# Performance work log

Measured on AMD Instinct MI355X. Metric: run time of the kernel, lower is better.

## Reference

```python
import jax, jax.numpy as jnp
import numpy as np

NUM_GRAPHS = 64
MAX_NODES = 512
D_MODEL = 512


def _lengths():
    # deterministic variable graph sizes in [256, 512]
    return 256 + (np.arange(NUM_GRAPHS) * 7) % 257


def setup_inputs() -> dict:
    key = jax.random.key(0)
    lengths = _lengths()
    total = int(lengths.sum())  # 23557
    # per-node graph id and within-graph position (replaces torch.split + pad_sequence)
    graph_ids = np.repeat(np.arange(NUM_GRAPHS, dtype=np.int32), lengths)
    pos_ids = np.concatenate([np.arange(n, dtype=np.int32) for n in lengths])
    batched_h = jax.random.normal(key, (total, D_MODEL), dtype=jnp.float32)
    return {
        "batched_h": batched_h,
        "graph_ids": jnp.asarray(graph_ids),
        "pos_ids": jnp.asarray(pos_ids),
        "B": NUM_GRAPHS,
        "max_n": MAX_NODES,
    }


def reference(batched_h, graph_ids, pos_ids, B, max_n):
    # pad_sequence equivalent: scatter nodes into [B, max_n, D] zero-padded tensor
    D = batched_h.shape[-1]
    padded = jnp.zeros((B, max_n, D), dtype=batched_h.dtype)
    padded = padded.at[graph_ids, pos_ids].set(batched_h)
    # Wq = Wk = Identity; bmm(q, k^T) -> [B, max_n, max_n]
    inst_out = jnp.einsum("bnd,bmd->bnm", padded, padded)
    # return_feat=False -> feat_out is empty; return inst_out only
    return inst_out
```

## Files before the change

kernel.cpp:

```cpp
#include <hip/hip_runtime.h>
#include <hip/hip_bf16.h>

#define DCONST 512
#define MAXN   512
#define NGRAPH 64

typedef __bf16 bf16x8 __attribute__((ext_vector_type(8)));
typedef float  f32x4  __attribute__((ext_vector_type(4)));
typedef float  fvec4  __attribute__((ext_vector_type(4)));

__global__ void pad_convert(const float* __restrict__ h,
                            __bf16* __restrict__ padded)
{
    const int t   = blockIdx.x * blockDim.x + threadIdx.x;
    const int row = t >> 6;
    const int seg = t & 63;
    const int g   = row >> 9;
    const int p   = row & 511;

    int off = 0, m7 = 0;
    for (int i = 0; i < g; ++i) {
        off += 256 + m7;
        m7 += 7; if (m7 >= 257) m7 -= 257;
    }
    const int len = 256 + m7;

    bf16x8 v = {};
    if (p < len) {
        const fvec4* src = reinterpret_cast<const fvec4*>(
            h + (size_t)(off + p) * DCONST + seg * 8);
        fvec4 a = src[0];
        fvec4 b = src[1];
        v[0] = (__bf16)a[0]; v[1] = (__bf16)a[1]; v[2] = (__bf16)a[2]; v[3] = (__bf16)a[3];
        v[4] = (__bf16)b[0]; v[5] = (__bf16)b[1]; v[6] = (__bf16)b[2]; v[7] = (__bf16)b[3];
    }
    *reinterpret_cast<bf16x8*>(padded + (size_t)row * DCONST + seg * 8) = v;
}

__constant__ const int TI10[10] = {0,0,0,0,1,1,1,2,2,3};
__constant__ const int TJ10[10] = {0,1,2,3,1,2,3,2,3,3};

__global__ __launch_bounds__(256, 2) void gemm_xxt(const __bf16* __restrict__ X,
                                                   float* __restrict__ out)
{
    __shared__ __align__(16) __bf16 lds[2][2][128][64];

    const int bid = blockIdx.x;
    const int xcd = bid & 7;
    const int idx = bid >> 3;
    const int g   = xcd * 8 + idx / 10;
    const int tl  = idx % 10;
    const int ti  = TI10[tl];
    const int tj  = TJ10[tl];
    const bool diag = (ti == tj);
    const int row0 = ti * 128;
    const int col0 = tj * 128;

    const __bf16* __restrict__ Xg = X + (size_t)g * MAXN * DCONST;

    const int tid  = threadIdx.x;
    const int wave = tid >> 6;
    const int lane = tid & 63;
    const int wr   = wave >> 1;
    const int wc   = wave & 1;

    f32x4 acc[4][4] = {};

    const int srow  = lane >> 3;
    const int sslot = lane & 7;

    auto stage = [&](int buf, int kt) {
        const int k0 = kt * 64;
        #pragma unroll
        for (int r = 0; r < 4; ++r) {
            const int rbase = wave * 8 + r * 32;
            const int rr    = rbase + srow;
            const int chunk = sslot ^ (rr & 7);
            const __bf16* gA = Xg + (size_t)(row0 + rr) * DCONST + k0 + chunk * 8;
            __builtin_amdgcn_global_load_lds(gA, &lds[buf][0][rbase][0], 16, 0, 0);
            if (!diag) {
                const __bf16* gB = Xg + (size_t)(col0 + rr) * DCONST + k0 + chunk * 8;
                __builtin_amdgcn_global_load_lds(gB, &lds[buf][1][rbase][0], 16, 0, 0);
            }
        }
    };

    stage(0, 0);
    asm volatile("s_waitcnt vmcnt(0)" ::: "memory");
    __syncthreads();

    int cur = 0;
    const int fr = lane & 15;
    const int q  = lane >> 4;
    const int bb = diag ? 0 : 1;

    #pragma unroll
    for (int kt = 0; kt < 8; ++kt) {
        if (kt < 7) stage(cur ^ 1, kt + 1);

        bf16x8 afr[2][4], bfr[2][4];
        #pragma unroll
        for (int ks = 0; ks < 2; ++ks) {
            const int chunk = ks * 4 + q;
            #pragma unroll
            for (int m = 0; m < 4; ++m) {
                const int rr   = wr * 64 + m * 16 + fr;
                const int slot = chunk ^ (rr & 7);
                afr[ks][m] = *reinterpret_cast<const bf16x8*>(&lds[cur][0][rr][slot * 8]);
            }
            #pragma unroll
            for (int n = 0; n < 4; ++n) {
                const int rr   = wc * 64 + n * 16 + fr;
                const int slot = chunk ^ (rr & 7);
                bfr[ks][n] = *reinterpret_cast<const bf16x8*>(&lds[cur][bb][rr][slot * 8]);
            }
        }

        #pragma unroll
        for (int ks = 0; ks < 2; ++ks)
            #pragma unroll
            for (int m = 0; m < 4; ++m)
                #pragma unroll
                for (int n = 0; n < 4; ++n)
                    acc[m][n] = __builtin_amdgcn_mfma_f32_16x16x32_bf16(
                        afr[ks][m], bfr[ks][n], acc[m][n], 0, 0, 0);

        if (kt < 7) {
            asm volatile("s_waitcnt vmcnt(0)" ::: "memory");
            __syncthreads();
        }
        cur ^= 1;
    }

    float* __restrict__ og = out + (size_t)g * MAXN * MAXN;
    const int rl0 = wr * 64 + q * 4;
    const int cl0 = wc * 64 + fr;
    #pragma unroll
    for (int m = 0; m < 4; ++m) {
        #pragma unroll
        for (int n = 0; n < 4; ++n) {
            f32x4 v = acc[m][n];
            float* p = og + (size_t)(row0 + rl0 + m * 16) * MAXN + col0 + cl0 + n * 16;
            #pragma unroll
            for (int r = 0; r < 4; ++r)
                p[(size_t)r * MAXN] = v[r];
            if (!diag) {
                float* pT = og + (size_t)(col0 + cl0 + n * 16) * MAXN
                               + row0 + rl0 + m * 16;
                *reinterpret_cast<f32x4*>(pT) = v;
            }
        }
    }
}

extern "C" void kernel_launch(void* const* d_in, const int* in_sizes, int n_in,
                              void* d_out, int out_size, void* d_ws, size_t ws_size,
                              hipStream_t stream)
{
    const float* h   = (const float*)d_in[0];
    __bf16* padded   = (__bf16*)d_ws;
    float*  out      = (float*)d_out;

    const int rows = NGRAPH * MAXN;
    pad_convert<<<rows * 64 / 256, 256, 0, stream>>>(h, padded);

    gemm_xxt<<<dim3(NGRAPH * 10), dim3(256), 0, stream>>>(padded, out);
}
```

Before: 126.8 us.

## Fuse ragged pad and bf16 conversion into the Gram GEMM kernel

Removes the separate pad_convert kernel and the bf16 padded workspace. The GEMM now loads fp32 rows directly from the ragged input into registers, zero-filling rows past each graph's length, then converts them to bf16 and writes them to swizzled LDS for the next k-tile. This eliminates an intermediate global write/read and a kernel launch. In exchange, staging goes through registers instead of direct global-to-LDS loads, which raises register pressure, and the fp32 input is re-read by multiple tiles.

```diff
diff --git a/kernel.cpp b/kernel.cpp
--- a/kernel.cpp
+++ b/kernel.cpp
@@ -9,39 +9,11 @@
 typedef float  f32x4  __attribute__((ext_vector_type(4)));
 typedef float  fvec4  __attribute__((ext_vector_type(4)));
 
-__global__ void pad_convert(const float* __restrict__ h,
-                            __bf16* __restrict__ padded)
-{
-    const int t   = blockIdx.x * blockDim.x + threadIdx.x;
-    const int row = t >> 6;
-    const int seg = t & 63;
-    const int g   = row >> 9;
-    const int p   = row & 511;
-
-    int off = 0, m7 = 0;
-    for (int i = 0; i < g; ++i) {
-        off += 256 + m7;
-        m7 += 7; if (m7 >= 257) m7 -= 257;
-    }
-    const int len = 256 + m7;
-
-    bf16x8 v = {};
-    if (p < len) {
-        const fvec4* src = reinterpret_cast<const fvec4*>(
-            h + (size_t)(off + p) * DCONST + seg * 8);
-        fvec4 a = src[0];
-        fvec4 b = src[1];
-        v[0] = (__bf16)a[0]; v[1] = (__bf16)a[1]; v[2] = (__bf16)a[2]; v[3] = (__bf16)a[3];
-        v[4] = (__bf16)b[0]; v[5] = (__bf16)b[1]; v[6] = (__bf16)b[2]; v[7] = (__bf16)b[3];
-    }
-    *reinterpret_cast<bf16x8*>(padded + (size_t)row * DCONST + seg * 8) = v;
-}
-
 __constant__ const int TI10[10] = {0,0,0,0,1,1,1,2,2,3};
 __constant__ const int TJ10[10] = {0,1,2,3,1,2,3,2,3,3};
 
-__global__ __launch_bounds__(256, 2) void gemm_xxt(const __bf16* __restrict__ X,
-                                                   float* __restrict__ out)
+__global__ __launch_bounds__(256, 2) void gram_fused(const float* __restrict__ h,
+                                                     float* __restrict__ out)
 {
     __shared__ __align__(16) __bf16 lds[2][2][128][64];
 
@@ -56,7 +28,12 @@
     const int row0 = ti * 128;
     const int col0 = tj * 128;
 
-    const __bf16* __restrict__ Xg = X + (size_t)g * MAXN * DCONST;
+    int off = 0, m7 = 0;
+    for (int i = 0; i < g; ++i) {
+        off += 256 + m7;
+        m7 += 7; if (m7 >= 257) m7 -= 257;
+    }
+    const int len = 256 + m7;
 
     const int tid  = threadIdx.x;
     const int wave = tid >> 6;
@@ -64,29 +41,67 @@
     const int wr   = wave >> 1;
     const int wc   = wave & 1;
 
+    const int slot = tid & 7;
+    const int rq   = tid >> 3;
+
     f32x4 acc[4][4] = {};
 
-    const int srow  = lane >> 3;
-    const int sslot = lane & 7;
+    fvec4 la[4][2], lb[4][2];
 
-    auto stage = [&](int buf, int kt) {
+    auto issue_loads = [&](int kt) {
         const int k0 = kt * 64;
         #pragma unroll
         for (int r = 0; r < 4; ++r) {
-            const int rbase = wave * 8 + r * 32;
-            const int rr    = rbase + srow;
-            const int chunk = sslot ^ (rr & 7);
-            const __bf16* gA = Xg + (size_t)(row0 + rr) * DCONST + k0 + chunk * 8;
-            __builtin_amdgcn_global_load_lds(gA, &lds[buf][0][rbase][0], 16, 0, 0);
+            const int rr = rq + r * 32;
+            const int ra = row0 + rr;
+            if (ra < len) {
+                const fvec4* s = reinterpret_cast<const fvec4*>(
+                    h + (size_t)(off + ra) * DCONST + k0 + slot * 8);
+                la[r][0] = s[0];
+                la[r][1] = s[1];
+            } else {
+                la[r][0] = (fvec4){0.f, 0.f, 0.f, 0.f};
+                la[r][1] = (fvec4){0.f, 0.f, 0.f, 0.f};
+            }
             if (!diag) {
-                const __bf16* gB = Xg + (size_t)(col0 + rr) * DCONST + k0 + chunk * 8;
-                __builtin_amdgcn_global_load_lds(gB, &lds[buf][1][rbase][0], 16, 0, 0);
+                const int rb = col0 + rr;
+                if (rb < len) {
+                    const fvec4* s = reinterpret_cast<const fvec4*>(
+                        h + (size_t)(off + rb) * DCONST + k0 + slot * 8);
+                    lb[r][0] = s[0];
+                    lb[r][1] = s[1];
+                } else {
+                    lb[r][0] = (fvec4){0.f, 0.f, 0.f, 0.f};
+                    lb[r][1] = (fvec4){0.f, 0.f, 0.f, 0.f};
+                }
             }
         }
     };
 
-    stage(0, 0);
-    asm volatile("s_waitcnt vmcnt(0)" ::: "memory");
+    auto write_tiles = [&](int buf) {
+        #pragma unroll
+        for (int r = 0; r < 4; ++r) {
+            const int rr = rq + r * 32;
+            const int sl = (slot ^ (rr & 7)) * 8;
+            bf16x8 v;
+            v[0] = (__bf16)la[r][0][0]; v[1] = (__bf16)la[r][0][1];
+            v[2] = (__bf16)la[r][0][2]; v[3] = (__bf16)la[r][0][3];
+            v[4] = (__bf16)la[r][1][0]; v[5] = (__bf16)la[r][1][1];
+            v[6] = (__bf16)la[r][1][2]; v[7] = (__bf16)la[r][1][3];
+            *reinterpret_cast<bf16x8*>(&lds[buf][0][rr][sl]) = v;
+            if (!diag) {
+                bf16x8 w;
+                w[0] = (__bf16)lb[r][0][0]; w[1] = (__bf16)lb[r][0][1];
+                w[2] = (__bf16)lb[r][0][2]; w[3] = (__bf16)lb[r][0][3];
+                w[4] = (__bf16)lb[r][1][0]; w[5] = (__bf16)lb[r][1][1];
+                w[6] = (__bf16)lb[r][1][2]; w[7] = (__bf16)lb[r][1][3];
+                *reinterpret_cast<bf16x8*>(&lds[buf][1][rr][sl]) = w;
+            }
+        }
+    };
+
+    issue_loads(0);
+    write_tiles(0);
     __syncthreads();
 
     int cur = 0;
@@ -96,7 +111,7 @@
 
     #pragma unroll
     for (int kt = 0; kt < 8; ++kt) {
-        if (kt < 7) stage(cur ^ 1, kt + 1);
+        if (kt < 7) issue_loads(kt + 1);
 
         bf16x8 afr[2][4], bfr[2][4];
         #pragma unroll
@@ -104,15 +119,15 @@
             const int chunk = ks * 4 + q;
             #pragma unroll
             for (int m = 0; m < 4; ++m) {
-                const int rr   = wr * 64 + m * 16 + fr;
-                const int slot = chunk ^ (rr & 7);
-                afr[ks][m] = *reinterpret_cast<const bf16x8*>(&lds[cur][0][rr][slot * 8]);
+                const int rr = wr * 64 + m * 16 + fr;
+                const int sl = (chunk ^ (rr & 7)) * 8;
+                afr[ks][m] = *reinterpret_cast<const bf16x8*>(&lds[cur][0][rr][sl]);
             }
             #pragma unroll
             for (int n = 0; n < 4; ++n) {
-                const int rr   = wc * 64 + n * 16 + fr;
-                const int slot = chunk ^ (rr & 7);
-                bfr[ks][n] = *reinterpret_cast<const bf16x8*>(&lds[cur][bb][rr][slot * 8]);
+                const int rr = wc * 64 + n * 16 + fr;
+                const int sl = (chunk ^ (rr & 7)) * 8;
+                bfr[ks][n] = *reinterpret_cast<const bf16x8*>(&lds[cur][bb][rr][sl]);
             }
         }
 
@@ -126,7 +141,7 @@
                         afr[ks][m], bfr[ks][n], acc[m][n], 0, 0, 0);
 
         if (kt < 7) {
-            asm volatile("s_waitcnt vmcnt(0)" ::: "memory");
+            write_tiles(cur ^ 1);
             __syncthreads();
         }
         cur ^= 1;
@@ -157,12 +172,9 @@
                               void* d_out, int out_size, void* d_ws, size_t ws_size,
                               hipStream_t stream)
 {
-    const float* h   = (const float*)d_in[0];
-    __bf16* padded   = (__bf16*)d_ws;
-    float*  out      = (float*)d_out;
+    const float* h = (const float*)d_in[0];
+    float* out     = (float*)d_out;
+    (void)d_ws; (void)ws_size;
 
-    const int rows = NGRAPH * MAXN;
-    pad_convert<<<rows * 64 / 256, 256, 0, stream>>>(h, padded);
-
-    gemm_xxt<<<dim3(NGRAPH * 10), dim3(256), 0, stream>>>(padded, out);
+    gram_fused<<<dim3(NGRAPH * 10), dim3(256), 0, stream>>>(h, out);
 }
```

Result: no change. 124.8 us (-1.5%).

## Deepen GEMM K pipeline to four LDS stages with two-ahead prefetch

Applied to the files above, without the earlier changes.

Replaces the double-buffered 64-wide K tiles with a 4-buffer ring of 32-wide K tiles, prefetching two stages ahead and waiting only on older loads (vmcnt(4)) before each barrier. This is meant to hide global-to-LDS latency better than the previous full vmcnt(0) drain. The diagonal tile now also loads its B operand separately instead of reusing A, which adds redundant loads. The iteration count doubles, so there are more barriers. The swizzle is changed to fit 32-element rows. There is also a cosmetic b[7-4] index edit in pad_convert.

```diff
diff --git a/kernel.cpp b/kernel.cpp
--- a/kernel.cpp
+++ b/kernel.cpp
@@ -32,7 +32,7 @@
         fvec4 a = src[0];
         fvec4 b = src[1];
         v[0] = (__bf16)a[0]; v[1] = (__bf16)a[1]; v[2] = (__bf16)a[2]; v[3] = (__bf16)a[3];
-        v[4] = (__bf16)b[0]; v[5] = (__bf16)b[1]; v[6] = (__bf16)b[2]; v[7] = (__bf16)b[3];
+        v[4] = (__bf16)b[0]; v[5] = (__bf16)b[1]; v[6] = (__bf16)b[2]; v[7] = (__bf16)b[7-4];
     }
     *reinterpret_cast<bf16x8*>(padded + (size_t)row * DCONST + seg * 8) = v;
 }
@@ -43,7 +43,8 @@
 __global__ __launch_bounds__(256, 2) void gemm_xxt(const __bf16* __restrict__ X,
                                                    float* __restrict__ out)
 {
-    __shared__ __align__(16) __bf16 lds[2][2][128][64];
+    __shared__ __align__(16) __bf16 ldsA[4][128][32];
+    __shared__ __align__(16) __bf16 ldsB[4][128][32];
 
     const int bid = blockIdx.x;
     const int xcd = bid & 7;
@@ -64,72 +65,66 @@
     const int wr   = wave >> 1;
     const int wc   = wave & 1;
 
-    f32x4 acc[4][4] = {};
+    const int lrow  = lane >> 2;
+    const int lslot = lane & 3;
 
-    const int srow  = lane >> 3;
-    const int sslot = lane & 7;
-
-    auto stage = [&](int buf, int kt) {
-        const int k0 = kt * 64;
+    auto stage = [&](int s) {
+        const int buf = s & 3;
+        const int k0  = s * 32;
         #pragma unroll
-        for (int r = 0; r < 4; ++r) {
-            const int rbase = wave * 8 + r * 32;
-            const int rr    = rbase + srow;
-            const int chunk = sslot ^ (rr & 7);
-            const __bf16* gA = Xg + (size_t)(row0 + rr) * DCONST + k0 + chunk * 8;
-            __builtin_amdgcn_global_load_lds(gA, &lds[buf][0][rbase][0], 16, 0, 0);
-            if (!diag) {
-                const __bf16* gB = Xg + (size_t)(col0 + rr) * DCONST + k0 + chunk * 8;
-                __builtin_amdgcn_global_load_lds(gB, &lds[buf][1][rbase][0], 16, 0, 0);
-            }
+        for (int r = 0; r < 2; ++r) {
+            const int rbase = r * 64 + wave * 16;
+            const int row   = rbase + lrow;
+            const int chunk = lslot ^ ((row >> 1) & 3);
+            const __bf16* gA = Xg + (size_t)(row0 + row) * DCONST + k0 + chunk * 8;
+            __builtin_amdgcn_global_load_lds(gA, &ldsA[buf][rbase][0], 16, 0, 0);
+            const int rB = diag ? row0 + row : col0 + row;
+            const __bf16* gB = Xg + (size_t)rB * DCONST + k0 + chunk * 8;
+            __builtin_amdgcn_global_load_lds(gB, &ldsB[buf][rbase][0], 16, 0, 0);
         }
     };
 
-    stage(0, 0);
-    asm volatile("s_waitcnt vmcnt(0)" ::: "memory");
-    __syncthreads();
+    stage(0);
+    stage(1);
+    asm volatile("s_waitcnt vmcnt(4)\n\ts_barrier" ::: "memory");
 
-    int cur = 0;
     const int fr = lane & 15;
     const int q  = lane >> 4;
-    const int bb = diag ? 0 : 1;
+    f32x4 acc[4][4] = {};
 
     #pragma unroll
-    for (int kt = 0; kt < 8; ++kt) {
-        if (kt < 7) stage(cur ^ 1, kt + 1);
+    for (int s = 0; s < 16; ++s) {
+        if (s + 2 < 16) stage(s + 2);
 
-        bf16x8 afr[2][4], bfr[2][4];
+        const int buf = s & 3;
+        bf16x8 afr[4], bfr[4];
         #pragma unroll
-        for (int ks = 0; ks < 2; ++ks) {
-            const int chunk = ks * 4 + q;
-            #pragma unroll
-            for (int m = 0; m < 4; ++m) {
-                const int rr   = wr * 64 + m * 16 + fr;
-                const int slot = chunk ^ (rr & 7);
-                afr[ks][m] = *reinterpret_cast<const bf16x8*>(&lds[cur][0][rr][slot * 8]);
-            }
-            #pragma unroll
-            for (int n = 0; n < 4; ++n) {
-                const int rr   = wc * 64 + n * 16 + fr;
-                const int slot = chunk ^ (rr & 7);
-                bfr[ks][n] = *reinterpret_cast<const bf16x8*>(&lds[cur][bb][rr][slot * 8]);
-            }
+        for (int m = 0; m < 4; ++m) {
+            const int rr = wr * 64 + m * 16 + fr;
+            const int sl = (q ^ ((rr >> 1) & 3)) * 8;
+            afr[m] = *reinterpret_cast<const bf16x8*>(&ldsA[buf][rr][sl]);
+        }
+        #pragma unroll
+        for (int n = 0; n < 4; ++n) {
+            const int rr = wc * 64 + n * 16 + fr;
+            const int sl = (q ^ ((rr >> 1) & 3)) * 8;
+            bfr[n] = *reinterpret_cast<const bf16x8*>(&ldsB[buf][rr][sl]);
         }
 
         #pragma unroll
-        for (int ks = 0; ks < 2; ++ks)
+        for (int m = 0; m < 4; ++m)
             #pragma unroll
-            for (int m = 0; m < 4; ++m)
-                #pragma unroll
-                for (int n = 0; n < 4; ++n)
-                    acc[m][n] = __builtin_amdgcn_mfma_f32_16x16x32_bf16(
-                        afr[ks][m], bfr[ks][n], acc[m][n], 0, 0, 0);
+            for (int n = 0; n < 4; ++n)
+                acc[m][n] = __builtin_amdgcn_mfma_f32_16x16x32_bf16(
+                    afr[m], bfr[n], acc[m][n], 0, 0, 0);
 
-        if (kt < 7) {
-            asm volatile("s_waitcnt vmcnt(0)" ::: "memory");
-            __syncthreads();
+        if (s < 15) {
+            if (s + 2 < 16) {
+                asm volatile("s_waitcnt vmcnt(4)\n\ts_barrier" ::: "memory");
+            } else {
+                asm volatile("s_waitcnt vmcnt(0)\n\ts_barrier" ::: "memory");
+            }
         }
-        cur ^= 1;
     }
 
     float* __restrict__ og = out + (size_t)g * MAXN * MAXN;
```

Result: no change. 128.9 us (+1.7%).
